# Kernel tuning notes

Measured on AMD Instinct MI355X. Metric: run time of the kernel, lower is better.

Reference implementation:

```python
import jax, jax.numpy as jnp
import numpy as np

KH = KW = 3
K = KH * KW
PAD = 1  # SAME padding, stride 1, dilation 1 -> pad = (k-1)//2 = 1


def _bilinear_gather(x, py, px):
    """Bilinear sample x [B,H,W,C] at float coords (py,px) [B,P] with zero padding."""
    B, H, W, C = x.shape
    y0 = jnp.floor(py)
    x0 = jnp.floor(px)
    y1 = y0 + 1.0
    x1 = x0 + 1.0
    wy1 = py - y0
    wx1 = px - x0
    wy0 = 1.0 - wy1
    wx0 = 1.0 - wx1
    xf = x.reshape(B, H * W, C)

    def gather(yi, xi):
        valid = (yi >= 0) & (yi <= H - 1) & (xi >= 0) & (xi <= W - 1)
        yc = jnp.clip(yi, 0, H - 1).astype(jnp.int32)
        xc = jnp.clip(xi, 0, W - 1).astype(jnp.int32)
        idx = yc * W + xc  # [B,P]
        v = jnp.take_along_axis(xf, idx[..., None], axis=1)  # [B,P,C]
        return v * valid[..., None].astype(x.dtype)

    return (gather(y0, x0) * (wy0 * wx0)[..., None]
            + gather(y0, x1) * (wy0 * wx1)[..., None]
            + gather(y1, x0) * (wy1 * wx0)[..., None]
            + gather(y1, x1) * (wy1 * wx1)[..., None])


def setup_inputs() -> dict:
    key = jax.random.key(0)
    k1, k2, k3, k4, k5 = jax.random.split(key, 5)
    B, H, W, Cin, Cout = 4, 128, 128, 64, 64
    x = jax.random.normal(k1, (B, H, W, Cin), dtype=jnp.float32)
    kernel = jax.random.normal(k2, (KH, KW, Cin, Cout), dtype=jnp.float32) * 0.05
    bias = jax.random.normal(k3, (Cout,), dtype=jnp.float32) * 0.05
    # offset/mask-producing conv (zeros-initialized in training; small random here)
    offset_kernel = jax.random.normal(k4, (KH, KW, Cin, 3 * K), dtype=jnp.float32) * 0.01
    offset_bias = jax.random.normal(k5, (3 * K,), dtype=jnp.float32) * 0.01
    return {"x": x, "kernel": kernel, "bias": bias,
            "offset_kernel": offset_kernel, "offset_bias": offset_bias}


def reference(x, kernel, bias, offset_kernel, offset_bias):
    B, H, W, C = x.shape
    # offset/mask branch: standard SAME conv
    om = jax.lax.conv_general_dilated(
        x, offset_kernel, window_strides=(1, 1), padding='SAME',
        dimension_numbers=('NHWC', 'HWIO', 'NHWC')) + offset_bias
    offset = om[..., :2 * K].reshape(B, H, W, K, 2)  # (dy, dx) per tap
    mask = jax.nn.sigmoid(om[..., 2 * K:])           # [B,H,W,K]
    dy = offset[..., 0]
    dx = offset[..., 1]
    # base sampling grid per output pixel / kernel tap
    ky, kx = jnp.meshgrid(jnp.arange(KH), jnp.arange(KW), indexing='ij')
    ky = ky.reshape(-1).astype(x.dtype)  # [K]
    kx = kx.reshape(-1).astype(x.dtype)
    oy = jnp.arange(H, dtype=x.dtype)[:, None, None]   # [H,1,1]
    ox = jnp.arange(W, dtype=x.dtype)[None, :, None]   # [1,W,1]
    py = oy - PAD + ky + dy  # [B,H,W,K]
    px = ox - PAD + kx + dx
    P = H * W * K
    sampled = _bilinear_gather(x, py.reshape(B, P), px.reshape(B, P))  # [B,P,C]
    sampled = sampled.reshape(B, H, W, K, C) * mask[..., None]
    w = kernel.reshape(K, C, -1)  # [K,Cin,Cout]
    out = jnp.einsum('bhwkc,kco->bhwo', sampled, w) + bias
    return out
```

## Files before the change

### kernel.cpp

```cpp
#include <hip/hip_runtime.h>
#include <hip/hip_bf16.h>
#include <math.h>

#define BB 4
#define HH 128
#define WW 128
#define CIN 64
#define COUT 64
#define KK 9
#define OMC 27
#define NPIX (BB * HH * WW)

typedef __attribute__((ext_vector_type(8))) short bf16x8;
typedef __attribute__((ext_vector_type(4))) float f32x4;

static __device__ __forceinline__ unsigned int pkcvt(float a, float b) {
    __hip_bfloat162 h = __float22bfloat162_rn(make_float2(a, b));
    return *reinterpret_cast<unsigned int*>(&h);
}
static __device__ __forceinline__ float bflo(unsigned int u) {
    return __uint_as_float(u << 16);
}
static __device__ __forceinline__ float bfhi(unsigned int u) {
    return __uint_as_float(u & 0xffff0000u);
}

__global__ __launch_bounds__(64) void weight_transform(
    const float* __restrict__ wmain, const float* __restrict__ wofs,
    uint4* __restrict__ wb, uint4* __restrict__ wf)
{
    const int tg = blockIdx.x * 64 + threadIdx.x;
    if (tg < 4608) {
        const int lane = tg & 63;
        const int nf   = (tg >> 6) & 3;
        const int ks   = tg >> 8;
        const int k0   = ks * 32 + ((lane >> 4) * 8);
        const int n    = nf * 16 + (lane & 15);
        uint4 q;
        q.x = pkcvt(wmain[(size_t)(k0 + 0) * COUT + n], wmain[(size_t)(k0 + 1) * COUT + n]);
        q.y = pkcvt(wmain[(size_t)(k0 + 2) * COUT + n], wmain[(size_t)(k0 + 3) * COUT + n]);
        q.z = pkcvt(wmain[(size_t)(k0 + 4) * COUT + n], wmain[(size_t)(k0 + 5) * COUT + n]);
        q.w = pkcvt(wmain[(size_t)(k0 + 6) * COUT + n], wmain[(size_t)(k0 + 7) * COUT + n]);
        wb[tg] = q;
    } else {
        const int idx  = tg - 4608;
        const int lane = idx & 63;
        const int frag = idx >> 6;
        const int nf   = frag & 1;
        const int ks   = frag >> 1;
        const int t    = ks >> 1;
        const int kw   = ks & 1;
        const int j    = nf * 16 + (lane & 15);
        const int c0   = kw * 32 + ((lane >> 4) * 8);
        uint4 q;
        if (j < OMC) {
            const float* wp = wofs + ((size_t)t * CIN + c0) * OMC + j;
            q.x = pkcvt(wp[0 * OMC], wp[1 * OMC]);
            q.y = pkcvt(wp[2 * OMC], wp[3 * OMC]);
            q.z = pkcvt(wp[4 * OMC], wp[5 * OMC]);
            q.w = pkcvt(wp[6 * OMC], wp[7 * OMC]);
        } else {
            q.x = q.y = q.z = q.w = 0u;
        }
        wf[frag * 64 + lane] = q;
    }
}

#define TMB 32

__global__ __launch_bounds__(256) void dcn_fused(
    const float* __restrict__ x,
    const uint4* __restrict__ wb,
    const uint4* __restrict__ wf,
    const float* __restrict__ bias,
    const float* __restrict__ bofs,
    float* __restrict__ out)
{
    __shared__ char shm[23040 + 3456 + 4608 + 4608 + 1152];
    char*   xs5   = shm;
    float*  om_s  = (float*)(shm + 23040);
    float4* ent_w = (float4*)(shm + 26496);
    int4*   ent_o = (int4*)(shm + 31104);
    int*    ent_f = (int*)(shm + 35712);
    f32x4*  om_red = (f32x4*)(shm + 26496);
    f32x4*  red    = (f32x4*)shm;

    const int tid  = threadIdx.x;
    const int lane = tid & 63;
    const int wv   = tid >> 6;
    const int pair = wv >> 1;
    const int kw   = wv & 1;
    const int bid  = ((blockIdx.x & 7) << 8) + (blockIdx.x >> 3);
    const int pix0 = bid * TMB;
    const int b    = pix0 >> 14;
    const int h    = (pix0 >> 7) & (HH - 1);
    const int w0   = pix0 & (WW - 1);
    const float* xb = x + (size_t)b * HH * WW * CIN;

    #pragma unroll
    for (int it = 0; it < 6; ++it) {
        const int idx = it * 256 + tid;
        if (idx < 1440) {
            const int c8   = idx & 7;
            const int cell = idx >> 3;
            const int ty   = cell / 36;
            const int wi   = cell - ty * 36;
            const int hy   = h - 2 + ty;
            const int wcol = w0 - 2 + wi;
            uint4 q;
            if ((unsigned)hy < (unsigned)HH && (unsigned)wcol < (unsigned)WW) {
                const float* p = xb + ((size_t)hy * WW + wcol) * CIN + c8 * 8;
                const float4 a0 = *(const float4*)p;
                const float4 a1 = *(const float4*)(p + 4);
                q.x = pkcvt(a0.x, a0.y);
                q.y = pkcvt(a0.z, a0.w);
                q.z = pkcvt(a1.x, a1.y);
                q.w = pkcvt(a1.z, a1.w);
            } else {
                q.x = q.y = q.z = q.w = 0u;
            }
            const int off = cell * 128 + ((c8 * 16) ^ ((cell & 7) << 4));
            *(uint4*)(xs5 + off) = q;
        }
    }
    __syncthreads();

    f32x4 accm[2] = {};
    #pragma unroll
    for (int t = 0; t < KK; ++t) {
        const int ty = t / 3, tx = t % 3;
        const int cell = (ty + 1) * 36 + (pair * 16 + (lane & 15) + tx + 1);
        const int aoff = cell * 128 + ((kw * 64 + (lane >> 4) * 16) ^ ((cell & 7) << 4));
        const bf16x8 a = *(const bf16x8*)(xs5 + aoff);
        const uint4* wf0 = wf + ((t * 2 + kw) * 2) * 64 + lane;
        const bf16x8 b0 = *(const bf16x8*)(wf0);
        const bf16x8 b1 = *(const bf16x8*)(wf0 + 64);
        accm[0] = __builtin_amdgcn_mfma_f32_16x16x32_bf16(a, b0, accm[0], 0, 0, 0);
        accm[1] = __builtin_amdgcn_mfma_f32_16x16x32_bf16(a, b1, accm[1], 0, 0, 0);
    }

    if (kw == 1) {
        om_red[(pair * 2 + 0) * 64 + lane] = accm[0];
        om_red[(pair * 2 + 1) * 64 + lane] = accm[1];
    }
    __syncthreads();
    if (kw == 0) {
        #pragma unroll
        for (int nf = 0; nf < 2; ++nf) {
            const int j = nf * 16 + (lane & 15);
            if (j >= OMC) continue;
            const f32x4 o = om_red[(pair * 2 + nf) * 64 + lane];
            const float bb = bofs[j];
            const int m0 = pair * 16 + ((lane >> 4) * 4);
            #pragma unroll
            for (int r = 0; r < 4; ++r) {
                float val = accm[nf][r] + o[r] + bb;
                const int wpix = w0 + m0 + r;
                if (j < 18) {
                    const int t = j >> 1;
                    if ((j & 1) == 0) val += (float)(h - 1 + t / 3);
                    else              val += (float)(wpix - 1 + t % 3);
                } else {
                    val = 1.0f / (1.0f + __expf(-val));
                }
                om_s[(m0 + r) * OMC + j] = val;
            }
        }
    }
    __syncthreads();

    for (int e = tid; e < 288; e += 256) {
        const int px = e / 9;
        const int t  = e - px * 9;
        const float py  = om_s[px * OMC + 2 * t];
        const float pxx = om_s[px * OMC + 2 * t + 1];
        const float mk  = om_s[px * OMC + 18 + t];

        const float fy = floorf(py), fx = floorf(pxx);
        const int y0 = (int)fy, x0 = (int)fx;
        const float wy1 = py - fy, wx1 = pxx - fx;
        const float wy0 = 1.0f - wy1, wx0 = 1.0f - wx1;
        const bool vy0 = (unsigned)y0 < (unsigned)HH;
        const bool vy1 = (unsigned)(y0 + 1) < (unsigned)HH;
        const bool vx0 = (unsigned)x0 < (unsigned)WW;
        const bool vx1 = (unsigned)(x0 + 1) < (unsigned)WW;
        float4 w4;
        w4.x = (vy0 && vx0) ? wy0 * wx0 * mk : 0.0f;
        w4.y = (vy0 && vx1) ? wy0 * wx1 * mk : 0.0f;
        w4.z = (vy1 && vx0) ? wy1 * wx0 * mk : 0.0f;
        w4.w = (vy1 && vx1) ? wy1 * wx1 * mk : 0.0f;

        const int r0  = y0 - (h - 2);
        const int c0i = x0 - (w0 - 2);
        int4 o4;
        int fl;
        if ((unsigned)r0 <= 3u && (unsigned)c0i <= 34u) {
            const int base = r0 * 36 + c0i;
            o4.x = base * 128;
            o4.y = (base + 1) * 128;
            o4.z = (base + 36) * 128;
            o4.w = (base + 37) * 128;
            fl = 0;
        } else {
            const int yc0 = min(max(y0, 0), HH - 1);
            const int yc1 = min(max(y0 + 1, 0), HH - 1);
            const int xc0 = min(max(x0, 0), WW - 1);
            const int xc1 = min(max(x0 + 1, 0), WW - 1);
            o4.x = (yc0 * WW + xc0) * (CIN * 4);
            o4.y = (yc0 * WW + xc1) * (CIN * 4);
            o4.z = (yc1 * WW + xc0) * (CIN * 4);
            o4.w = (yc1 * WW + xc1) * (CIN * 4);
            fl = 1;
        }
        ent_w[e] = w4;
        ent_o[e] = o4;
        ent_f[e] = fl;
    }
    __syncthreads();

    const int p   = lane & 15;
    const int g   = lane >> 4;
    const int kwg = kw * 64 + g * 16;
    const char* xg = (const char*)xb + (size_t)(kw * 32 + g * 8) * 4;
    const int ebase = pair * 144 + p * 9;

    f32x4 acc[4] = {};

    #pragma unroll
    for (int t = 0; t < KK; ++t) {
        const float4 w4 = ent_w[ebase + t];
        const int4   o4 = ent_o[ebase + t];
        float s[8];
        if (ent_f[ebase + t] == 0) {
            const uint4 q0 = *(const uint4*)(xs5 + o4.x + (kwg ^ ((o4.x >> 3) & 0x70)));
            const uint4 q1 = *(const uint4*)(xs5 + o4.y + (kwg ^ ((o4.y >> 3) & 0x70)));
            const uint4 q2 = *(const uint4*)(xs5 + o4.z + (kwg ^ ((o4.z >> 3) & 0x70)));
            const uint4 q3 = *(const uint4*)(xs5 + o4.w + (kwg ^ ((o4.w >> 3) & 0x70)));
            const unsigned int* u0 = (const unsigned int*)&q0;
            const unsigned int* u1 = (const unsigned int*)&q1;
            const unsigned int* u2 = (const unsigned int*)&q2;
            const unsigned int* u3 = (const unsigned int*)&q3;
            #pragma unroll
            for (int i = 0; i < 4; ++i) {
                s[2 * i]     = w4.x * bflo(u0[i]) + w4.y * bflo(u1[i])
                             + w4.z * bflo(u2[i]) + w4.w * bflo(u3[i]);
                s[2 * i + 1] = w4.x * bfhi(u0[i]) + w4.y * bfhi(u1[i])
                             + w4.z * bfhi(u2[i]) + w4.w * bfhi(u3[i]);
            }
        } else {
            const float4 c0a = *(const float4*)(xg + o4.x);
            const float4 c0b = *(const float4*)(xg + o4.x + 16);
            const float4 c1a = *(const float4*)(xg + o4.y);
            const float4 c1b = *(const float4*)(xg + o4.y + 16);
            const float4 c2a = *(const float4*)(xg + o4.z);
            const float4 c2b = *(const float4*)(xg + o4.z + 16);
            const float4 c3a = *(const float4*)(xg + o4.w);
            const float4 c3b = *(const float4*)(xg + o4.w + 16);
            #pragma unroll
            for (int i = 0; i < 4; ++i) {
                s[i]     = w4.x * ((const float*)&c0a)[i] + w4.y * ((const float*)&c1a)[i]
                         + w4.z * ((const float*)&c2a)[i] + w4.w * ((const float*)&c3a)[i];
                s[4 + i] = w4.x * ((const float*)&c0b)[i] + w4.y * ((const float*)&c1b)[i]
                         + w4.z * ((const float*)&c2b)[i] + w4.w * ((const float*)&c3b)[i];
            }
        }

        uint4 aq;
        aq.x = pkcvt(s[0], s[1]);
        aq.y = pkcvt(s[2], s[3]);
        aq.z = pkcvt(s[4], s[5]);
        aq.w = pkcvt(s[6], s[7]);
        const bf16x8 a = *(const bf16x8*)&aq;

        const uint4* wb0 = wb + ((t * 2 + kw) * 4) * 64 + lane;
        const bf16x8 b0 = *(const bf16x8*)(wb0 + 0 * 64);
        const bf16x8 b1 = *(const bf16x8*)(wb0 + 1 * 64);
        const bf16x8 b2 = *(const bf16x8*)(wb0 + 2 * 64);
        const bf16x8 b3 = *(const bf16x8*)(wb0 + 3 * 64);
        acc[0] = __builtin_amdgcn_mfma_f32_16x16x32_bf16(a, b0, acc[0], 0, 0, 0);
        acc[1] = __builtin_amdgcn_mfma_f32_16x16x32_bf16(a, b1, acc[1], 0, 0, 0);
        acc[2] = __builtin_amdgcn_mfma_f32_16x16x32_bf16(a, b2, acc[2], 0, 0, 0);
        acc[3] = __builtin_amdgcn_mfma_f32_16x16x32_bf16(a, b3, acc[3], 0, 0, 0);
    }

    __syncthreads();
    if (kw == 1) {
        #pragma unroll
        for (int nf = 0; nf < 4; ++nf) red[(pair * 4 + nf) * 64 + lane] = acc[nf];
    }
    __syncthreads();
    if (kw == 0) {
        #pragma unroll
        for (int nf = 0; nf < 4; ++nf) {
            const f32x4 o = red[(pair * 4 + nf) * 64 + lane];
            const int n  = nf * 16 + (lane & 15);
            const float bs = bias[n];
            const int m0 = pair * 16 + ((lane >> 4) * 4);
            #pragma unroll
            for (int r = 0; r < 4; ++r) {
                out[(size_t)(pix0 + m0 + r) * COUT + n] = acc[nf][r] + o[r] + bs;
            }
        }
    }
}

extern "C" void kernel_launch(void* const* d_in, const int* in_sizes, int n_in,
                              void* d_out, int out_size, void* d_ws, size_t ws_size,
                              hipStream_t stream)
{
    const float* x     = (const float*)d_in[0];
    const float* wmain = (const float*)d_in[1];
    const float* bias  = (const float*)d_in[2];
    const float* wofs  = (const float*)d_in[3];
    const float* bofs  = (const float*)d_in[4];
    float* out = (float*)d_out;
    uint4* wb  = (uint4*)d_ws;
    uint4* wf  = (uint4*)((char*)d_ws + 73728);

    weight_transform<<<108, 64, 0, stream>>>(wmain, wofs, wb, wf);
    dcn_fused<<<NPIX / TMB, 256, 0, stream>>>(x, wb, wf, bias, bofs, out);
}
```

Before: 38.41 us.

## Compute sampling entries per lane inline and drop offset-conv split-K reduction

```diff
diff --git a/kernel.cpp b/kernel.cpp
--- a/kernel.cpp
+++ b/kernel.cpp
@@ -76,14 +76,10 @@
     const float* __restrict__ bofs,
     float* __restrict__ out)
 {
-    __shared__ char shm[23040 + 3456 + 4608 + 4608 + 1152];
+    __shared__ char shm[23040 + 3456];
     char*   xs5   = shm;
     float*  om_s  = (float*)(shm + 23040);
-    float4* ent_w = (float4*)(shm + 26496);
-    int4*   ent_o = (int4*)(shm + 31104);
-    int*    ent_f = (int*)(shm + 35712);
-    f32x4*  om_red = (f32x4*)(shm + 26496);
-    f32x4*  red    = (f32x4*)shm;
+    f32x4*  red   = (f32x4*)shm;
 
     const int tid  = threadIdx.x;
     const int lane = tid & 63;
@@ -130,31 +126,29 @@
     for (int t = 0; t < KK; ++t) {
         const int ty = t / 3, tx = t % 3;
         const int cell = (ty + 1) * 36 + (pair * 16 + (lane & 15) + tx + 1);
-        const int aoff = cell * 128 + ((kw * 64 + (lane >> 4) * 16) ^ ((cell & 7) << 4));
-        const bf16x8 a = *(const bf16x8*)(xs5 + aoff);
-        const uint4* wf0 = wf + ((t * 2 + kw) * 2) * 64 + lane;
-        const bf16x8 b0 = *(const bf16x8*)(wf0);
-        const bf16x8 b1 = *(const bf16x8*)(wf0 + 64);
-        accm[0] = __builtin_amdgcn_mfma_f32_16x16x32_bf16(a, b0, accm[0], 0, 0, 0);
-        accm[1] = __builtin_amdgcn_mfma_f32_16x16x32_bf16(a, b1, accm[1], 0, 0, 0);
-    }
-
-    if (kw == 1) {
-        om_red[(pair * 2 + 0) * 64 + lane] = accm[0];
-        om_red[(pair * 2 + 1) * 64 + lane] = accm[1];
-    }
-    __syncthreads();
+        const int swz  = (cell & 7) << 4;
+        #pragma unroll
+        for (int ch2 = 0; ch2 < 2; ++ch2) {
+            const int aoff = cell * 128 + ((ch2 * 64 + (lane >> 4) * 16) ^ swz);
+            const bf16x8 a = *(const bf16x8*)(xs5 + aoff);
+            const uint4* wf0 = wf + ((t * 2 + ch2) * 2) * 64 + lane;
+            const bf16x8 b0 = *(const bf16x8*)(wf0);
+            const bf16x8 b1 = *(const bf16x8*)(wf0 + 64);
+            accm[0] = __builtin_amdgcn_mfma_f32_16x16x32_bf16(a, b0, accm[0], 0, 0, 0);
+            accm[1] = __builtin_amdgcn_mfma_f32_16x16x32_bf16(a, b1, accm[1], 0, 0, 0);
+        }
+    }
+
     if (kw == 0) {
         #pragma unroll
         for (int nf = 0; nf < 2; ++nf) {
             const int j = nf * 16 + (lane & 15);
             if (j >= OMC) continue;
-            const f32x4 o = om_red[(pair * 2 + nf) * 64 + lane];
             const float bb = bofs[j];
             const int m0 = pair * 16 + ((lane >> 4) * 4);
             #pragma unroll
             for (int r = 0; r < 4; ++r) {
-                float val = accm[nf][r] + o[r] + bb;
+                float val = accm[nf][r] + bb;
                 const int wpix = w0 + m0 + r;
                 if (j < 18) {
                     const int t = j >> 1;
@@ -169,99 +163,79 @@
     }
     __syncthreads();
 
-    for (int e = tid; e < 288; e += 256) {
-        const int px = e / 9;
-        const int t  = e - px * 9;
-        const float py  = om_s[px * OMC + 2 * t];
-        const float pxx = om_s[px * OMC + 2 * t + 1];
-        const float mk  = om_s[px * OMC + 18 + t];
+    const int p   = lane & 15;
+    const int g   = lane >> 4;
+    const int kwg = kw * 64 + g * 16;
+    const char* xg = (const char*)xb + (size_t)(kw * 32 + g * 8) * 4;
+    const float* omp = om_s + (pair * 16 + p) * OMC;
+
+    f32x4 acc[4] = {};
+
+    #pragma unroll
+    for (int t = 0; t < KK; ++t) {
+        const float py  = omp[2 * t];
+        const float pxx = omp[2 * t + 1];
+        const float mk  = omp[18 + t];
 
         const float fy = floorf(py), fx = floorf(pxx);
-        const int y0 = (int)fy, x0 = (int)fx;
+        const int y0  = (int)fy, x0i = (int)fx;
         const float wy1 = py - fy, wx1 = pxx - fx;
         const float wy0 = 1.0f - wy1, wx0 = 1.0f - wx1;
         const bool vy0 = (unsigned)y0 < (unsigned)HH;
         const bool vy1 = (unsigned)(y0 + 1) < (unsigned)HH;
-        const bool vx0 = (unsigned)x0 < (unsigned)WW;
-        const bool vx1 = (unsigned)(x0 + 1) < (unsigned)WW;
-        float4 w4;
-        w4.x = (vy0 && vx0) ? wy0 * wx0 * mk : 0.0f;
-        w4.y = (vy0 && vx1) ? wy0 * wx1 * mk : 0.0f;
-        w4.z = (vy1 && vx0) ? wy1 * wx0 * mk : 0.0f;
-        w4.w = (vy1 && vx1) ? wy1 * wx1 * mk : 0.0f;
-
+        const bool vx0 = (unsigned)x0i < (unsigned)WW;
+        const bool vx1 = (unsigned)(x0i + 1) < (unsigned)WW;
+        const float w00 = (vy0 && vx0) ? wy0 * wx0 * mk : 0.0f;
+        const float w01 = (vy0 && vx1) ? wy0 * wx1 * mk : 0.0f;
+        const float w10 = (vy1 && vx0) ? wy1 * wx0 * mk : 0.0f;
+        const float w11 = (vy1 && vx1) ? wy1 * wx1 * mk : 0.0f;
         const int r0  = y0 - (h - 2);
-        const int c0i = x0 - (w0 - 2);
-        int4 o4;
-        int fl;
+        const int c0i = x0i - (w0 - 2);
+
+        float s[8];
         if ((unsigned)r0 <= 3u && (unsigned)c0i <= 34u) {
-            const int base = r0 * 36 + c0i;
-            o4.x = base * 128;
-            o4.y = (base + 1) * 128;
-            o4.z = (base + 36) * 128;
-            o4.w = (base + 37) * 128;
-            fl = 0;
-        } else {
-            const int yc0 = min(max(y0, 0), HH - 1);
-            const int yc1 = min(max(y0 + 1, 0), HH - 1);
-            const int xc0 = min(max(x0, 0), WW - 1);
-            const int xc1 = min(max(x0 + 1, 0), WW - 1);
-            o4.x = (yc0 * WW + xc0) * (CIN * 4);
-            o4.y = (yc0 * WW + xc1) * (CIN * 4);
-            o4.z = (yc1 * WW + xc0) * (CIN * 4);
-            o4.w = (yc1 * WW + xc1) * (CIN * 4);
-            fl = 1;
-        }
-        ent_w[e] = w4;
-        ent_o[e] = o4;
-        ent_f[e] = fl;
-    }
-    __syncthreads();
-
-    const int p   = lane & 15;
-    const int g   = lane >> 4;
-    const int kwg = kw * 64 + g * 16;
-    const char* xg = (const char*)xb + (size_t)(kw * 32 + g * 8) * 4;
-    const int ebase = pair * 144 + p * 9;
-
-    f32x4 acc[4] = {};
-
-    #pragma unroll
-    for (int t = 0; t < KK; ++t) {
-        const float4 w4 = ent_w[ebase + t];
-        const int4   o4 = ent_o[ebase + t];
-        float s[8];
-        if (ent_f[ebase + t] == 0) {
-            const uint4 q0 = *(const uint4*)(xs5 + o4.x + (kwg ^ ((o4.x >> 3) & 0x70)));
-            const uint4 q1 = *(const uint4*)(xs5 + o4.y + (kwg ^ ((o4.y >> 3) & 0x70)));
-            const uint4 q2 = *(const uint4*)(xs5 + o4.z + (kwg ^ ((o4.z >> 3) & 0x70)));
-            const uint4 q3 = *(const uint4*)(xs5 + o4.w + (kwg ^ ((o4.w >> 3) & 0x70)));
+            const int ib = (r0 * 36 + c0i) * 128;
+            const int i1 = ib + 128;
+            const int i2 = ib + 36 * 128;
+            const int i3 = ib + 37 * 128;
+            const uint4 q0 = *(const uint4*)(xs5 + ib + (kwg ^ ((ib >> 3) & 0x70)));
+            const uint4 q1 = *(const uint4*)(xs5 + i1 + (kwg ^ ((i1 >> 3) & 0x70)));
+            const uint4 q2 = *(const uint4*)(xs5 + i2 + (kwg ^ ((i2 >> 3) & 0x70)));
+            const uint4 q3 = *(const uint4*)(xs5 + i3 + (kwg ^ ((i3 >> 3) & 0x70)));
             const unsigned int* u0 = (const unsigned int*)&q0;
             const unsigned int* u1 = (const unsigned int*)&q1;
             const unsigned int* u2 = (const unsigned int*)&q2;
             const unsigned int* u3 = (const unsigned int*)&q3;
             #pragma unroll
             for (int i = 0; i < 4; ++i) {
-                s[2 * i]     = w4.x * bflo(u0[i]) + w4.y * bflo(u1[i])
-                             + w4.z * bflo(u2[i]) + w4.w * bflo(u3[i]);
-                s[2 * i + 1] = w4.x * bfhi(u0[i]) + w4.y * bfhi(u1[i])
-                             + w4.z * bfhi(u2[i]) + w4.w * bfhi(u3[i]);
+                s[2 * i]     = w00 * bflo(u0[i]) + w01 * bflo(u1[i])
+                             + w10 * bflo(u2[i]) + w11 * bflo(u3[i]);
+                s[2 * i + 1] = w00 * bfhi(u0[i]) + w01 * bfhi(u1[i])
+                             + w10 * bfhi(u2[i]) + w11 * bfhi(u3[i]);
             }
         } else {
-            const float4 c0a = *(const float4*)(xg + o4.x);
-            const float4 c0b = *(const float4*)(xg + o4.x + 16);
-            const float4 c1a = *(const float4*)(xg + o4.y);
-            const float4 c1b = *(const float4*)(xg + o4.y + 16);
-            const float4 c2a = *(const float4*)(xg + o4.z);
-            const float4 c2b = *(const float4*)(xg + o4.z + 16);
-            const float4 c3a = *(const float4*)(xg + o4.w);
-            const float4 c3b = *(const float4*)(xg + o4.w + 16);
+            const int yc0 = min(max(y0, 0), HH - 1);
+            const int yc1 = min(max(y0 + 1, 0), HH - 1);
+            const int xc0 = min(max(x0i, 0), WW - 1);
+            const int xc1 = min(max(x0i + 1, 0), WW - 1);
+            const int o0 = (yc0 * WW + xc0) * (CIN * 4);
+            const int o1 = (yc0 * WW + xc1) * (CIN * 4);
+            const int o2 = (yc1 * WW + xc0) * (CIN * 4);
+            const int o3 = (yc1 * WW + xc1) * (CIN * 4);
+            const float4 c0a = *(const float4*)(xg + o0);
+            const float4 c0b = *(const float4*)(xg + o0 + 16);
+            const float4 c1a = *(const float4*)(xg + o1);
+            const float4 c1b = *(const float4*)(xg + o1 + 16);
+            const float4 c2a = *(const float4*)(xg + o2);
+            const float4 c2b = *(const float4*)(xg + o2 + 16);
+            const float4 c3a = *(const float4*)(xg + o3);
+            const float4 c3b = *(const float4*)(xg + o3 + 16);
             #pragma unroll
             for (int i = 0; i < 4; ++i) {
-                s[i]     = w4.x * ((const float*)&c0a)[i] + w4.y * ((const float*)&c1a)[i]
-                         + w4.z * ((const float*)&c2a)[i] + w4.w * ((const float*)&c3a)[i];
-                s[4 + i] = w4.x * ((const float*)&c0b)[i] + w4.y * ((const float*)&c1b)[i]
-                         + w4.z * ((const float*)&c2b)[i] + w4.w * ((const float*)&c3b)[i];
+                s[i]     = w00 * ((const float*)&c0a)[i] + w01 * ((const float*)&c1a)[i]
+                         + w10 * ((const float*)&c2a)[i] + w11 * ((const float*)&c3a)[i];
+                s[4 + i] = w00 * ((const float*)&c0b)[i] + w01 * ((const float*)&c1b)[i]
+                         + w10 * ((const float*)&c2b)[i] + w11 * ((const float*)&c3b)[i];
             }
         }
 
```

After: 39.92 us. +3.9%, slower.
